# Optimization experiments

Measured on AMD Instinct MI355X. Metric: run time of the kernel, lower is better.

The kernel has to match this reference:

```python
import jax, jax.numpy as jnp
import numpy as np

B, S, H, NH = 1, 2048, 1024, 16
HD = H // NH
LAYER_NUMBER = 1
EPS = 1e-5
NEG_INF = -1e9


def _layernorm(x, g, b):
    mu = jnp.mean(x, axis=-1, keepdims=True)
    var = jnp.mean((x - mu) ** 2, axis=-1, keepdims=True)
    return (x - mu) * jax.lax.rsqrt(var + EPS) * g + b


def _bloom_gelu(x):
    # tanh approximation used by Megatron/Bloom
    return x * 0.5 * (1.0 + jnp.tanh(0.79788456 * x * (1.0 + 0.044715 * x * x)))


def setup_inputs() -> dict:
    key = jax.random.key(0)
    ks = jax.random.split(key, 8)

    def w(k, shape, scale=0.02):
        return jax.random.normal(k, shape, jnp.float32) * scale

    # additive causal mask: 0 where attended, -1e9 where masked
    causal = jnp.where(jnp.tril(jnp.ones((S, S), bool)), 0.0, NEG_INF).astype(jnp.float32)
    attention_mask = causal[None, None]  # [1,1,S,S]

    return {
        "hidden_states": jax.random.normal(ks[0], (B, S, H), jnp.float32),
        "attention_mask": attention_mask,
        "alibi": w(ks[1], (B * NH, 1, S), 1.0),
        "ln1_g": jnp.ones((H,), jnp.float32),
        "ln1_b": jnp.zeros((H,), jnp.float32),
        "qkv_w": w(ks[2], (3 * H, H)),
        "qkv_b": jnp.zeros((3 * H,), jnp.float32),
        "dense_w": w(ks[3], (H, H)),
        "dense_b": jnp.zeros((H,), jnp.float32),
        "ln2_g": jnp.ones((H,), jnp.float32),
        "ln2_b": jnp.zeros((H,), jnp.float32),
        "fc1_w": w(ks[4], (4 * H, H)),
        "fc1_b": jnp.zeros((4 * H,), jnp.float32),
        "fc2_w": w(ks[5], (H, 4 * H)),
        "fc2_b": jnp.zeros((H,), jnp.float32),
    }


def reference(hidden_states, attention_mask, alibi,
              ln1_g, ln1_b, qkv_w, qkv_b, dense_w, dense_b,
              ln2_g, ln2_b, fc1_w, fc1_b, fc2_w, fc2_b):
    dtype = hidden_states.dtype
    norm_factor = np.sqrt(HD).astype(np.float32) * LAYER_NUMBER
    beta = 1.0 / LAYER_NUMBER

    # --- input layernorm (residual = pre-LN hidden states) ---
    ln_out = _layernorm(hidden_states, ln1_g, ln1_b)
    residual = hidden_states

    # --- attention ---
    fused = ln_out @ qkv_w.T + qkv_b                      # [B,S,3H]
    fused = fused.reshape(B, S, NH, 3 * HD)
    q, k, v = fused[..., :HD], fused[..., HD:2 * HD], fused[..., 2 * HD:]

    scores = jnp.einsum('bqhd,bkhd->bhqk', q, k) / norm_factor \
             + beta * alibi.reshape(B, NH, 1, S)          # [B,NH,S,S]
    attn = scores * LAYER_NUMBER + attention_mask
    attn = jnp.maximum(attn, jnp.finfo(attn.dtype).min)
    probs = jax.nn.softmax(attn.astype(jnp.float32), axis=-1).astype(dtype)
    probs = probs * (attention_mask == 0.0)               # zero out masked positions

    ctx = jnp.einsum('bhqk,bkhd->bqhd', probs, v).reshape(B, S, H)
    attn_out = ctx @ dense_w.T + dense_b + residual       # dropout_add, p=0

    # --- post-attention layernorm + MLP ---
    ln2_out = _layernorm(attn_out, ln2_g, ln2_b)
    residual2 = attn_out
    h = _bloom_gelu(ln2_out @ fc1_w.T + fc1_b)            # [B,S,4H]
    out = h @ fc2_w.T + fc2_b + residual2                 # dropout_add, p=0
    return out
```

## Files before the change

kernel.cpp:

```cpp
#include <hip/hip_runtime.h>
#include <hip/hip_bf16.h>

typedef unsigned short u16;
typedef __attribute__((ext_vector_type(8))) short bf16x8;
typedef __attribute__((ext_vector_type(4))) float f32x4;

typedef __attribute__((address_space(1))) const void cgvoid;
typedef __attribute__((address_space(3))) void lvoid;

static __device__ __forceinline__ u16 f2bf(float x) {
    __hip_bfloat16 h = __float2bfloat16(x);
    return __builtin_bit_cast(u16, h);
}
static __device__ __forceinline__ float bf2f(u16 x) {
    return __builtin_bit_cast(float, ((unsigned)x) << 16);
}

static __device__ __forceinline__ void gload_lds16(const u16* g, u16* l) {
    __builtin_amdgcn_global_load_lds((cgvoid*)g, (lvoid*)l, 16, 0, 0);
}

__global__ __launch_bounds__(256) void prep(
    const float* __restrict__ hidden, const float* __restrict__ g1,
    const float* __restrict__ b1, u16* __restrict__ ln_out,
    const float* __restrict__ qkv_w, const float* __restrict__ dense_w,
    const float* __restrict__ fc1_w, const float* __restrict__ fc2_w,
    u16* __restrict__ qkv_wb, u16* __restrict__ dense_wb,
    u16* __restrict__ fc1_wb, u16* __restrict__ fc2_wb)
{
    const int t = threadIdx.x;
    if (blockIdx.x < 2048) {
        const int row = blockIdx.x;
        const float4 v = ((const float4*)(hidden + (size_t)row * 1024))[t];
        float s  = v.x + v.y + v.z + v.w;
        float sq = v.x*v.x + v.y*v.y + v.z*v.z + v.w*v.w;
#pragma unroll
        for (int d = 1; d < 64; d <<= 1) {
            s  += __shfl_xor(s, d, 64);
            sq += __shfl_xor(sq, d, 64);
        }
        __shared__ float ss[4], ssq[4];
        const int wave = t >> 6, lane = t & 63;
        if (lane == 0) { ss[wave] = s; ssq[wave] = sq; }
        __syncthreads();
        s  = ss[0] + ss[1] + ss[2] + ss[3];
        sq = ssq[0] + ssq[1] + ssq[2] + ssq[3];
        const float mu = s * (1.f / 1024.f);
        const float rinv = rsqrtf(sq * (1.f / 1024.f) - mu * mu + 1e-5f);
        const float4 gv = ((const float4*)g1)[t];
        const float4 bv = ((const float4*)b1)[t];
        ushort4 pk;
        pk.x = f2bf((v.x - mu) * rinv * gv.x + bv.x);
        pk.y = f2bf((v.y - mu) * rinv * gv.y + bv.y);
        pk.z = f2bf((v.z - mu) * rinv * gv.z + bv.z);
        pk.w = f2bf((v.w - mu) * rinv * gv.w + bv.w);
        ((ushort4*)(ln_out + (size_t)row * 1024))[t] = pk;
        return;
    }
    constexpr int C0 = 786432;
    constexpr int C1 = C0 + 262144;
    constexpr int C2 = C1 + 1048576;
    constexpr int C3 = C2 + 1048576;
    int i = (blockIdx.x - 2048) * 256 + t;
    const int stride = (gridDim.x - 2048) * 256;
    for (; i < C3; i += stride) {
        const float* src; u16* dst; int j;
        if (i < C0)      { src = qkv_w;   dst = qkv_wb;   j = i; }
        else if (i < C1) { src = dense_w; dst = dense_wb; j = i - C0; }
        else if (i < C2) { src = fc1_w;   dst = fc1_wb;   j = i - C1; }
        else             { src = fc2_w;   dst = fc2_wb;   j = i - C2; }
        const float4 v = ((const float4*)src)[j];
        ushort4 pk;
        pk.x = f2bf(v.x); pk.y = f2bf(v.y); pk.z = f2bf(v.z); pk.w = f2bf(v.w);
        ((ushort4*)dst)[j] = pk;
    }
}

template<int EPI, int BM, int BN>
__global__ __launch_bounds__(256, (BN == 128) ? 3 : 4) void gemm_bt(
    const u16* __restrict__ A, const u16* __restrict__ Bw,
    const float* __restrict__ bias, void* __restrict__ Cout,
    u16* __restrict__ p0, u16* __restrict__ pext,
    u16* __restrict__ kPo, u16* __restrict__ vPo,
    int M, int N, int K, int Kspan)
{
    constexpr int WC = BN / 64;
    constexpr int WR = 4 / WC;
    constexpr int MI = BM / (WR * 16);
    constexpr int NI = 4;
    __shared__ __align__(16) u16 As[BM * 64];
    __shared__ __align__(16) u16 Bs[BN * 64];
    const int t = threadIdx.x;
    const int lane = t & 63;
    const int wave = t >> 6;
    const int wr = wave / WC, wc = wave % WC;
    const int g = lane >> 4, r16 = lane & 15;

    const int nxy = gridDim.x * gridDim.y;
    const int bid0 = blockIdx.x + gridDim.x * blockIdx.y;
    const int v = (bid0 & 7) * (nxy >> 3) + (bid0 >> 3);
    const int tile_m = (v / gridDim.y) * BM;
    const int tile_n = (v % gridDim.y) * BN;
    const int kb = blockIdx.z * Kspan;

    f32x4 acc[MI][NI] = {};

    for (int k0 = kb; k0 < kb + Kspan; k0 += 64) {
        __syncthreads();
#pragma unroll
        for (int i = 0; i < BM / 32; ++i) {
            const int off = (t + i * 256) * 8;
            gload_lds16(A + (size_t)(tile_m + (off >> 6)) * K + k0 + (off & 63), As + off);
        }
#pragma unroll
        for (int i = 0; i < BN / 32; ++i) {
            const int off = (t + i * 256) * 8;
            gload_lds16(Bw + (size_t)(tile_n + (off >> 6)) * K + k0 + (off & 63), Bs + off);
        }
        __syncthreads();

        bf16x8 af[MI][2], bfr[NI][2];
#pragma unroll
        for (int mi = 0; mi < MI; ++mi)
#pragma unroll
            for (int ks = 0; ks < 2; ++ks)
                af[mi][ks] = *(const bf16x8*)(As + (wr*(MI*16) + mi*16 + r16)*64 + ks*32 + g*8);
#pragma unroll
        for (int ni = 0; ni < NI; ++ni)
#pragma unroll
            for (int ks = 0; ks < 2; ++ks)
                bfr[ni][ks] = *(const bf16x8*)(Bs + (wc*64 + ni*16 + r16)*64 + ks*32 + g*8);
#pragma unroll
        for (int mi = 0; mi < MI; ++mi)
#pragma unroll
            for (int ni = 0; ni < NI; ++ni) {
                acc[mi][ni] = __builtin_amdgcn_mfma_f32_16x16x32_bf16(af[mi][0], bfr[ni][0], acc[mi][ni], 0, 0, 0);
                acc[mi][ni] = __builtin_amdgcn_mfma_f32_16x16x32_bf16(af[mi][1], bfr[ni][1], acc[mi][ni], 0, 0, 0);
            }
    }

    u16* dst = nullptr;
    if constexpr (EPI == 4)
        dst = (blockIdx.z == 0) ? p0 : pext + (size_t)(blockIdx.z - 1) * ((size_t)M * N);

#pragma unroll
    for (int mi = 0; mi < MI; ++mi) {
#pragma unroll
        for (int ni = 0; ni < NI; ++ni) {
            const int col = tile_n + wc*64 + ni*16 + r16;
            const int row0 = tile_m + wr*(MI*16) + mi*16 + g*4;
            float vv[4];
#pragma unroll
            for (int r = 0; r < 4; ++r) {
                if constexpr (EPI == 4) vv[r] = acc[mi][ni][r];
                else                    vv[r] = acc[mi][ni][r] + bias[col];
            }
#pragma unroll
            for (int r = 0; r < 4; ++r) {
                const int row = row0 + r;
                if constexpr (EPI == 4) {
                    dst[(size_t)row * N + col] = f2bf(vv[r]);
                } else if constexpr (EPI == 0 || EPI == 3) {
                    ((u16*)Cout)[(size_t)row * N + col] = f2bf(vv[r]);
                } else {
                    const float c = 0.79788456f * vv[r] * (1.0f + 0.044715f * vv[r] * vv[r]);
                    ((u16*)Cout)[(size_t)row * N + col] = f2bf(vv[r] / (1.0f + __expf(-2.0f * c)));
                }
            }
            if constexpr (EPI == 3) {
                const int h = col / 192;
                const int fm = col % 192;
                if ((fm >> 6) == 1) {
                    const int f = fm - 64;
                    const int ks = f >> 5, gg = (f >> 3) & 3, e = f & 7;
#pragma unroll
                    for (int r = 0; r < 4; ++r) {
                        const int tkn = row0 + r;
                        const int kt = tkn >> 6, w = tkn & 63;
                        const int kn = ((w >> 5) << 1) | ((w >> 2) & 1);
                        const int rp = ((w >> 3) & 3) * 4 + (w & 3);
                        kPo[((size_t)(h*32 + kt))*4096 + (kn*2 + ks)*512 + (gg*16 + rp)*8 + e] = f2bf(vv[r]);
                    }
                } else if ((fm >> 6) == 2) {
                    const int f = fm - 128;
                    const int nd = f >> 4, rv = f & 15;
                    const int kt = row0 >> 6, w = row0 & 63;
                    const int ks = w >> 5, gg = (w >> 3) & 3, e0 = w & 7;
                    ushort4 pk4;
                    pk4.x = f2bf(vv[0]); pk4.y = f2bf(vv[1]);
                    pk4.z = f2bf(vv[2]); pk4.w = f2bf(vv[3]);
                    *(ushort4*)(vPo + ((size_t)(h*32 + kt))*4096 + (nd*2 + ks)*512 + (gg*16 + rv)*8 + e0) = pk4;
                }
            }
        }
    }
}

__global__ __launch_bounds__(256) void reduce2_ln(
    const u16* __restrict__ p0, const u16* __restrict__ p1,
    const float* __restrict__ bias, const float* __restrict__ res,
    float* __restrict__ attn_o, const float* __restrict__ g2,
    const float* __restrict__ b2, u16* __restrict__ ln_out)
{
    const int row = blockIdx.x;
    const int t = threadIdx.x;
    const size_t i = (size_t)row * 256 + t;
    const ushort4 a0 = ((const ushort4*)p0)[i];
    const ushort4 a1 = ((const ushort4*)p1)[i];
    const float4 bv = ((const float4*)bias)[t];
    const float4 rv = ((const float4*)res)[i];
    float4 v;
    v.x = bf2f(a0.x) + bf2f(a1.x) + bv.x + rv.x;
    v.y = bf2f(a0.y) + bf2f(a1.y) + bv.y + rv.y;
    v.z = bf2f(a0.z) + bf2f(a1.z) + bv.z + rv.z;
    v.w = bf2f(a0.w) + bf2f(a1.w) + bv.w + rv.w;
    ((float4*)attn_o)[i] = v;

    float s  = v.x + v.y + v.z + v.w;
    float sq = v.x*v.x + v.y*v.y + v.z*v.z + v.w*v.w;
#pragma unroll
    for (int d = 1; d < 64; d <<= 1) {
        s  += __shfl_xor(s, d, 64);
        sq += __shfl_xor(sq, d, 64);
    }
    __shared__ float ss[4], ssq[4];
    const int wave = t >> 6, lane = t & 63;
    if (lane == 0) { ss[wave] = s; ssq[wave] = sq; }
    __syncthreads();
    s  = ss[0] + ss[1] + ss[2] + ss[3];
    sq = ssq[0] + ssq[1] + ssq[2] + ssq[3];
    const float mu = s * (1.f / 1024.f);
    const float rinv = rsqrtf(sq * (1.f / 1024.f) - mu * mu + 1e-5f);
    const float4 gv = ((const float4*)g2)[t];
    const float4 b2v = ((const float4*)b2)[t];
    ushort4 pk;
    pk.x = f2bf((v.x - mu) * rinv * gv.x + b2v.x);
    pk.y = f2bf((v.y - mu) * rinv * gv.y + b2v.y);
    pk.z = f2bf((v.z - mu) * rinv * gv.z + b2v.z);
    pk.w = f2bf((v.w - mu) * rinv * gv.w + b2v.w);
    ((ushort4*)(ln_out + (size_t)row * 1024))[t] = pk;
}

template<int NP>
__global__ __launch_bounds__(256) void reduce_bias_res(
    const u16* __restrict__ p0, const u16* __restrict__ pext,
    const float* __restrict__ bias, const float* __restrict__ res,
    float* __restrict__ out, int n4, int n4row)
{
    int i = blockIdx.x * blockDim.x + threadIdx.x;
    const int stride = gridDim.x * blockDim.x;
    for (; i < n4; i += stride) {
        const ushort4 a0 = ((const ushort4*)p0)[i];
        float ax = bf2f(a0.x), ay = bf2f(a0.y), az = bf2f(a0.z), aw = bf2f(a0.w);
#pragma unroll
        for (int j = 0; j < NP - 1; ++j) {
            const ushort4 b = ((const ushort4*)pext)[(size_t)j * n4 + i];
            ax += bf2f(b.x); ay += bf2f(b.y); az += bf2f(b.z); aw += bf2f(b.w);
        }
        const float4 bv = ((const float4*)bias)[i & (n4row - 1)];
        const float4 rv = ((const float4*)res)[i];
        float4 o;
        o.x = ax + bv.x + rv.x;
        o.y = ay + bv.y + rv.y;
        o.z = az + bv.z + rv.z;
        o.w = aw + bv.w + rv.w;
        ((float4*)out)[i] = o;
    }
}

__global__ __launch_bounds__(256, 4) void attn_swapped(
    const u16* __restrict__ fused, const u16* __restrict__ kP,
    const u16* __restrict__ vP, const float* __restrict__ alibi,
    u16* __restrict__ ctx)
{
    const int bid = blockIdx.x;
    const int h = bid & 15;
    const int qt = 127 - (bid >> 4);
    const int qw0 = qt * 16;
    const int t = threadIdx.x;
    const int lane = t & 63, wave = t >> 6;
    const int g = lane >> 4, r16 = lane & 15;
    const int qrow = qw0 + r16;

    __shared__ float Ms[4][16], Ls[4][16];
    __shared__ float Os[4][4][16][17];

    const u16* qbase = fused + (size_t)qrow * 3072 + h * 192;
    bf16x8 qf[2];
    qf[0] = *(const bf16x8*)(qbase + g*8);
    qf[1] = *(const bf16x8*)(qbase + 32 + g*8);

    f32x4 o_acc[4] = {};
    float m_r = -3.0e38f, l_r = 0.f;

    const u16* kPh = kP + (size_t)h * 32 * 4096;
    const u16* vPh = vP + (size_t)h * 32 * 4096;
    const float* abase = alibi + (size_t)h * 2048;

    const int nkt = (qw0 >> 6) + 1;
    for (int kt = wave; kt < nkt; kt += 4) {
        const int kt0 = kt * 64;
        const u16* kT = kPh + (size_t)kt * 4096;
        const u16* vT = vPh + (size_t)kt * 4096;

        bf16x8 kf[4][2], vf[4][2];
#pragma unroll
        for (int kn = 0; kn < 4; ++kn) {
            kf[kn][0] = *(const bf16x8*)(kT + (kn*2 + 0)*512 + lane*8);
            kf[kn][1] = *(const bf16x8*)(kT + (kn*2 + 1)*512 + lane*8);
        }
        float4 al[4];
#pragma unroll
        for (int kn = 0; kn < 4; ++kn)
            al[kn] = *(const float4*)(abase + kt0 + 32*(kn>>1) + 8*g + 4*(kn&1));
#pragma unroll
        for (int nd = 0; nd < 4; ++nd) {
            vf[nd][0] = *(const bf16x8*)(vT + (nd*2 + 0)*512 + lane*8);
            vf[nd][1] = *(const bf16x8*)(vT + (nd*2 + 1)*512 + lane*8);
        }

        f32x4 sc[4] = {};
#pragma unroll
        for (int kn = 0; kn < 4; ++kn) {
            sc[kn] = __builtin_amdgcn_mfma_f32_16x16x32_bf16(kf[kn][0], qf[0], sc[kn], 0, 0, 0);
            sc[kn] = __builtin_amdgcn_mfma_f32_16x16x32_bf16(kf[kn][1], qf[1], sc[kn], 0, 0, 0);
        }

        float s[4][4];
        float rmax = -3.0e38f;
#pragma unroll
        for (int kn = 0; kn < 4; ++kn) {
            const int kb = kt0 + 32*(kn>>1) + 8*g + 4*(kn&1);
            const float alv[4] = {al[kn].x, al[kn].y, al[kn].z, al[kn].w};
#pragma unroll
            for (int r = 0; r < 4; ++r) {
                float v = sc[kn][r] * 0.125f + alv[r];
                v = (kb + r <= qrow) ? v : -1.0e30f;
                s[kn][r] = v;
                rmax = fmaxf(rmax, v);
            }
        }
        rmax = fmaxf(rmax, __shfl_xor(rmax, 16, 64));
        rmax = fmaxf(rmax, __shfl_xor(rmax, 32, 64));

        const float mnew = fmaxf(m_r, rmax);
        const float scale = __expf(m_r - mnew);
        m_r = mnew;

        float psum = 0.f;
        u16 ph[4][4];
#pragma unroll
        for (int kn = 0; kn < 4; ++kn)
#pragma unroll
            for (int r = 0; r < 4; ++r) {
                const float p = __expf(s[kn][r] - mnew);
                psum += p;
                ph[kn][r] = f2bf(p);
            }
        psum += __shfl_xor(psum, 16, 64);
        psum += __shfl_xor(psum, 32, 64);
        l_r = l_r * scale + psum;

#pragma unroll
        for (int nd = 0; nd < 4; ++nd)
#pragma unroll
            for (int r = 0; r < 4; ++r)
                o_acc[nd][r] *= scale;

        bf16x8 pf[2];
#pragma unroll
        for (int ks = 0; ks < 2; ++ks) {
            union { bf16x8 v; u16 e[8]; } u;
#pragma unroll
            for (int r = 0; r < 4; ++r) { u.e[r] = ph[2*ks][r]; u.e[4+r] = ph[2*ks+1][r]; }
            pf[ks] = u.v;
        }
#pragma unroll
        for (int nd = 0; nd < 4; ++nd) {
            o_acc[nd] = __builtin_amdgcn_mfma_f32_16x16x32_bf16(vf[nd][0], pf[0], o_acc[nd], 0, 0, 0);
            o_acc[nd] = __builtin_amdgcn_mfma_f32_16x16x32_bf16(vf[nd][1], pf[1], o_acc[nd], 0, 0, 0);
        }
    }

#pragma unroll
    for (int nd = 0; nd < 4; ++nd)
#pragma unroll
        for (int r = 0; r < 4; ++r)
            Os[wave][nd][g*4 + r][r16] = o_acc[nd][r];
    if (g == 0) { Ms[wave][r16] = m_r; Ls[wave][r16] = l_r; }
    __syncthreads();

    if (wave == 0) {
        const float m0 = Ms[0][r16], m1 = Ms[1][r16], m2 = Ms[2][r16], m3 = Ms[3][r16];
        const float ms = fmaxf(fmaxf(m0, m1), fmaxf(m2, m3));
        const float f0 = __expf(m0 - ms), f1 = __expf(m1 - ms);
        const float f2 = __expf(m2 - ms), f3 = __expf(m3 - ms);
        const float l = f0*Ls[0][r16] + f1*Ls[1][r16] + f2*Ls[2][r16] + f3*Ls[3][r16];
        const float inv = 1.0f / l;
#pragma unroll
        for (int nd = 0; nd < 4; ++nd) {
            float v[4];
#pragma unroll
            for (int r = 0; r < 4; ++r) {
                const int d = g*4 + r;
                v[r] = (f0*Os[0][nd][d][r16] + f1*Os[1][nd][d][r16] +
                        f2*Os[2][nd][d][r16] + f3*Os[3][nd][d][r16]) * inv;
            }
            ushort4 pk;
            pk.x = f2bf(v[0]); pk.y = f2bf(v[1]); pk.z = f2bf(v[2]); pk.w = f2bf(v[3]);
            *(ushort4*)(ctx + (size_t)qrow * 1024 + h*64 + nd*16 + g*4) = pk;
        }
    }
}

extern "C" void kernel_launch(void* const* d_in, const int* in_sizes, int n_in,
                              void* d_out, int out_size, void* d_ws, size_t ws_size,
                              hipStream_t stream)
{
    (void)in_sizes; (void)n_in; (void)out_size; (void)ws_size;
    const float* hidden  = (const float*)d_in[0];
    const float* alibi   = (const float*)d_in[2];
    const float* ln1_g   = (const float*)d_in[3];
    const float* ln1_b   = (const float*)d_in[4];
    const float* qkv_w   = (const float*)d_in[5];
    const float* qkv_b   = (const float*)d_in[6];
    const float* dense_w = (const float*)d_in[7];
    const float* dense_b = (const float*)d_in[8];
    const float* ln2_g   = (const float*)d_in[9];
    const float* ln2_b   = (const float*)d_in[10];
    const float* fc1_w   = (const float*)d_in[11];
    const float* fc1_b   = (const float*)d_in[12];
    const float* fc2_w   = (const float*)d_in[13];
    const float* fc2_b   = (const float*)d_in[14];
    float* out = (float*)d_out;

    char* p = (char*)d_ws;
    u16* ln_buf   = (u16*)p;  p += (size_t)2048 * 1024 * 2;
    u16* qkv_wb   = (u16*)p;  p += (size_t)3072 * 1024 * 2;
    u16* fusedq   = (u16*)p;  p += (size_t)2048 * 3072 * 2;
    u16* ctx      = (u16*)p;  p += (size_t)2048 * 1024 * 2;
    u16* dense_wb = (u16*)p;  p += (size_t)1024 * 1024 * 2;
    float* attn_o = (float*)p; p += (size_t)2048 * 1024 * 4;
    u16* fc1_wb   = (u16*)p;  p += (size_t)4096 * 1024 * 2;
    u16* fc2_wb   = (u16*)p;  p += (size_t)1024 * 4096 * 2;
    u16* pext     = (u16*)p;  p += (size_t)3 * 2048 * 1024 * 2;
    u16* part0    = (u16*)p;  p += (size_t)2048 * 1024 * 2;
    u16* hbuf = fusedq;
    u16* kP = (u16*)attn_o;
    u16* vP = kP + (size_t)16 * 32 * 4096;

    prep<<<6144, 256, 0, stream>>>(hidden, ln1_g, ln1_b, ln_buf,
                                   qkv_w, dense_w, fc1_w, fc2_w,
                                   qkv_wb, dense_wb, fc1_wb, fc2_wb);
    gemm_bt<3,128,64><<<dim3(16, 48), 256, 0, stream>>>(ln_buf, qkv_wb, qkv_b, fusedq,
                                                        nullptr, nullptr, kP, vP,
                                                        2048, 3072, 1024, 1024);
    attn_swapped<<<2048, 256, 0, stream>>>(fusedq, kP, vP, alibi, ctx);
    gemm_bt<4,128,64><<<dim3(16, 16, 2), 256, 0, stream>>>(ctx, dense_wb, nullptr, nullptr,
                                                           part0, pext, nullptr, nullptr,
                                                           2048, 1024, 1024, 512);
    reduce2_ln<<<2048, 256, 0, stream>>>(part0, pext, dense_b, hidden, attn_o,
                                         ln2_g, ln2_b, ln_buf);
    gemm_bt<2,128,128><<<dim3(16, 32), 256, 0, stream>>>(ln_buf, fc1_wb, fc1_b, hbuf,
                                                         nullptr, nullptr, nullptr, nullptr,
                                                         2048, 4096, 1024, 1024);
    gemm_bt<4,128,128><<<dim3(16, 8, 4), 256, 0, stream>>>(hbuf, fc2_wb, nullptr, nullptr,
                                                           part0, pext, nullptr, nullptr,
                                                           2048, 1024, 4096, 1024);
    reduce_bias_res<4><<<2048, 256, 0, stream>>>(part0, pext, fc2_b, attn_o, out,
                                                 2048*1024/4, 256);
}
```

Before: 157.4 us.

## Pair causal query tiles per attention block and pre-pack Q fragments

The attention kernel now handles two 16-row query tiles per block, one from the long end and one from the short end of the causal triangle, so every block does about the same work and the grid is halved. The QKV GEMM epilogue no longer writes the full fused row-major output. It scatters Q into an MFMA-fragment-packed layout, as K and V already were, so each Q fragment is read as one contiguous 16-byte load per lane and the dead fused Q/K/V store is gone. In exchange each block runs serially over both tiles with two extra syncthreads, and the epilogue's Q stores become scattered 2-byte writes.

```diff
diff --git a/kernel.cpp b/kernel.cpp
--- a/kernel.cpp
+++ b/kernel.cpp
@@ -81,7 +81,7 @@
     const u16* __restrict__ A, const u16* __restrict__ Bw,
     const float* __restrict__ bias, void* __restrict__ Cout,
     u16* __restrict__ p0, u16* __restrict__ pext,
-    u16* __restrict__ kPo, u16* __restrict__ vPo,
+    u16* __restrict__ qPo, u16* __restrict__ kPo, u16* __restrict__ vPo,
     int M, int N, int K, int Kspan)
 {
     constexpr int WC = BN / 64;
@@ -155,22 +155,32 @@
                 if constexpr (EPI == 4) vv[r] = acc[mi][ni][r];
                 else                    vv[r] = acc[mi][ni][r] + bias[col];
             }
-#pragma unroll
-            for (int r = 0; r < 4; ++r) {
-                const int row = row0 + r;
-                if constexpr (EPI == 4) {
-                    dst[(size_t)row * N + col] = f2bf(vv[r]);
-                } else if constexpr (EPI == 0 || EPI == 3) {
-                    ((u16*)Cout)[(size_t)row * N + col] = f2bf(vv[r]);
-                } else {
-                    const float c = 0.79788456f * vv[r] * (1.0f + 0.044715f * vv[r] * vv[r]);
-                    ((u16*)Cout)[(size_t)row * N + col] = f2bf(vv[r] / (1.0f + __expf(-2.0f * c)));
+            if constexpr (EPI != 3) {
+#pragma unroll
+                for (int r = 0; r < 4; ++r) {
+                    const int row = row0 + r;
+                    if constexpr (EPI == 4) {
+                        dst[(size_t)row * N + col] = f2bf(vv[r]);
+                    } else if constexpr (EPI == 0) {
+                        ((u16*)Cout)[(size_t)row * N + col] = f2bf(vv[r]);
+                    } else {
+                        const float c = 0.79788456f * vv[r] * (1.0f + 0.044715f * vv[r] * vv[r]);
+                        ((u16*)Cout)[(size_t)row * N + col] = f2bf(vv[r] / (1.0f + __expf(-2.0f * c)));
+                    }
                 }
-            }
-            if constexpr (EPI == 3) {
+            } else {
                 const int h = col / 192;
                 const int fm = col % 192;
-                if ((fm >> 6) == 1) {
+                if ((fm >> 6) == 0) {
+                    const int f = fm;
+                    const int ks = f >> 5, gg = (f >> 3) & 3, e = f & 7;
+#pragma unroll
+                    for (int r = 0; r < 4; ++r) {
+                        const int tkn = row0 + r;
+                        const int qt = tkn >> 4, rr = tkn & 15;
+                        qPo[((size_t)(h*128 + qt)*2 + ks)*512 + (gg*16 + rr)*8 + e] = f2bf(vv[r]);
+                    }
+                } else if ((fm >> 6) == 1) {
                     const int f = fm - 64;
                     const int ks = f >> 5, gg = (f >> 3) & 3, e = f & 7;
 #pragma unroll
@@ -181,7 +191,7 @@
                         const int rp = ((w >> 3) & 3) * 4 + (w & 3);
                         kPo[((size_t)(h*32 + kt))*4096 + (kn*2 + ks)*512 + (gg*16 + rp)*8 + e] = f2bf(vv[r]);
                     }
-                } else if ((fm >> 6) == 2) {
+                } else {
                     const int f = fm - 128;
                     const int nd = f >> 4, rv = f & 15;
                     const int kt = row0 >> 6, w = row0 & 63;
@@ -269,146 +279,151 @@
 }
 
 __global__ __launch_bounds__(256, 4) void attn_swapped(
-    const u16* __restrict__ fused, const u16* __restrict__ kP,
+    const u16* __restrict__ qP, const u16* __restrict__ kP,
     const u16* __restrict__ vP, const float* __restrict__ alibi,
     u16* __restrict__ ctx)
 {
     const int bid = blockIdx.x;
     const int h = bid & 15;
-    const int qt = 127 - (bid >> 4);
-    const int qw0 = qt * 16;
+    const int b = bid >> 4;
     const int t = threadIdx.x;
     const int lane = t & 63, wave = t >> 6;
     const int g = lane >> 4, r16 = lane & 15;
-    const int qrow = qw0 + r16;
 
     __shared__ float Ms[4][16], Ls[4][16];
     __shared__ float Os[4][4][16][17];
-
-    const u16* qbase = fused + (size_t)qrow * 3072 + h * 192;
-    bf16x8 qf[2];
-    qf[0] = *(const bf16x8*)(qbase + g*8);
-    qf[1] = *(const bf16x8*)(qbase + 32 + g*8);
-
-    f32x4 o_acc[4] = {};
-    float m_r = -3.0e38f, l_r = 0.f;
 
     const u16* kPh = kP + (size_t)h * 32 * 4096;
     const u16* vPh = vP + (size_t)h * 32 * 4096;
     const float* abase = alibi + (size_t)h * 2048;
 
-    const int nkt = (qw0 >> 6) + 1;
-    for (int kt = wave; kt < nkt; kt += 4) {
-        const int kt0 = kt * 64;
-        const u16* kT = kPh + (size_t)kt * 4096;
-        const u16* vT = vPh + (size_t)kt * 4096;
-
-        bf16x8 kf[4][2], vf[4][2];
-#pragma unroll
-        for (int kn = 0; kn < 4; ++kn) {
-            kf[kn][0] = *(const bf16x8*)(kT + (kn*2 + 0)*512 + lane*8);
-            kf[kn][1] = *(const bf16x8*)(kT + (kn*2 + 1)*512 + lane*8);
-        }
-        float4 al[4];
-#pragma unroll
-        for (int kn = 0; kn < 4; ++kn)
-            al[kn] = *(const float4*)(abase + kt0 + 32*(kn>>1) + 8*g + 4*(kn&1));
-#pragma unroll
-        for (int nd = 0; nd < 4; ++nd) {
-            vf[nd][0] = *(const bf16x8*)(vT + (nd*2 + 0)*512 + lane*8);
-            vf[nd][1] = *(const bf16x8*)(vT + (nd*2 + 1)*512 + lane*8);
-        }
-
-        f32x4 sc[4] = {};
-#pragma unroll
-        for (int kn = 0; kn < 4; ++kn) {
-            sc[kn] = __builtin_amdgcn_mfma_f32_16x16x32_bf16(kf[kn][0], qf[0], sc[kn], 0, 0, 0);
-            sc[kn] = __builtin_amdgcn_mfma_f32_16x16x32_bf16(kf[kn][1], qf[1], sc[kn], 0, 0, 0);
-        }
-
-        float s[4][4];
-        float rmax = -3.0e38f;
-#pragma unroll
-        for (int kn = 0; kn < 4; ++kn) {
-            const int kb = kt0 + 32*(kn>>1) + 8*g + 4*(kn&1);
-            const float alv[4] = {al[kn].x, al[kn].y, al[kn].z, al[kn].w};
-#pragma unroll
-            for (int r = 0; r < 4; ++r) {
-                float v = sc[kn][r] * 0.125f + alv[r];
-                v = (kb + r <= qrow) ? v : -1.0e30f;
-                s[kn][r] = v;
-                rmax = fmaxf(rmax, v);
-            }
-        }
-        rmax = fmaxf(rmax, __shfl_xor(rmax, 16, 64));
-        rmax = fmaxf(rmax, __shfl_xor(rmax, 32, 64));
-
-        const float mnew = fmaxf(m_r, rmax);
-        const float scale = __expf(m_r - mnew);
-        m_r = mnew;
-
-        float psum = 0.f;
-        u16 ph[4][4];
-#pragma unroll
-        for (int kn = 0; kn < 4; ++kn)
-#pragma unroll
-            for (int r = 0; r < 4; ++r) {
-                const float p = __expf(s[kn][r] - mnew);
-                psum += p;
-                ph[kn][r] = f2bf(p);
-            }
-        psum += __shfl_xor(psum, 16, 64);
-        psum += __shfl_xor(psum, 32, 64);
-        l_r = l_r * scale + psum;
-
+#pragma unroll
+    for (int half = 0; half < 2; ++half) {
+        const int qt = half ? b : (127 - b);
+        const int qw0 = qt * 16;
+        const int qrow = qw0 + r16;
+
+        bf16x8 qf[2];
+        qf[0] = *(const bf16x8*)(qP + ((size_t)(h*128 + qt)*2 + 0)*512 + lane*8);
+        qf[1] = *(const bf16x8*)(qP + ((size_t)(h*128 + qt)*2 + 1)*512 + lane*8);
+
+        f32x4 o_acc[4] = {};
+        float m_r = -3.0e38f, l_r = 0.f;
+
+        const int nkt = (qw0 >> 6) + 1;
+        for (int kt = wave; kt < nkt; kt += 4) {
+            const int kt0 = kt * 64;
+            const u16* kT = kPh + (size_t)kt * 4096;
+            const u16* vT = vPh + (size_t)kt * 4096;
+
+            bf16x8 kf[4][2], vf[4][2];
+#pragma unroll
+            for (int kn = 0; kn < 4; ++kn) {
+                kf[kn][0] = *(const bf16x8*)(kT + (kn*2 + 0)*512 + lane*8);
+                kf[kn][1] = *(const bf16x8*)(kT + (kn*2 + 1)*512 + lane*8);
+            }
+            float4 al[4];
+#pragma unroll
+            for (int kn = 0; kn < 4; ++kn)
+                al[kn] = *(const float4*)(abase + kt0 + 32*(kn>>1) + 8*g + 4*(kn&1));
+#pragma unroll
+            for (int nd = 0; nd < 4; ++nd) {
+                vf[nd][0] = *(const bf16x8*)(vT + (nd*2 + 0)*512 + lane*8);
+                vf[nd][1] = *(const bf16x8*)(vT + (nd*2 + 1)*512 + lane*8);
+            }
+
+            f32x4 sc[4] = {};
+#pragma unroll
+            for (int kn = 0; kn < 4; ++kn) {
+                sc[kn] = __builtin_amdgcn_mfma_f32_16x16x32_bf16(kf[kn][0], qf[0], sc[kn], 0, 0, 0);
+                sc[kn] = __builtin_amdgcn_mfma_f32_16x16x32_bf16(kf[kn][1], qf[1], sc[kn], 0, 0, 0);
+            }
+
+            float s[4][4];
+            float rmax = -3.0e38f;
+#pragma unroll
+            for (int kn = 0; kn < 4; ++kn) {
+                const int kb = kt0 + 32*(kn>>1) + 8*g + 4*(kn&1);
+                const float alv[4] = {al[kn].x, al[kn].y, al[kn].z, al[kn].w};
+#pragma unroll
+                for (int r = 0; r < 4; ++r) {
+                    float v = sc[kn][r] * 0.125f + alv[r];
+                    v = (kb + r <= qrow) ? v : -1.0e30f;
+                    s[kn][r] = v;
+                    rmax = fmaxf(rmax, v);
+                }
+            }
+            rmax = fmaxf(rmax, __shfl_xor(rmax, 16, 64));
+            rmax = fmaxf(rmax, __shfl_xor(rmax, 32, 64));
+
+            const float mnew = fmaxf(m_r, rmax);
+            const float scale = __expf(m_r - mnew);
+            m_r = mnew;
+
+            float psum = 0.f;
+            u16 ph[4][4];
+#pragma unroll
+            for (int kn = 0; kn < 4; ++kn)
+#pragma unroll
+                for (int r = 0; r < 4; ++r) {
+                    const float p = __expf(s[kn][r] - mnew);
+                    psum += p;
+                    ph[kn][r] = f2bf(p);
+                }
+            psum += __shfl_xor(psum, 16, 64);
+            psum += __shfl_xor(psum, 32, 64);
+            l_r = l_r * scale + psum;
+
+#pragma unroll
+            for (int nd = 0; nd < 4; ++nd)
+#pragma unroll
+                for (int r = 0; r < 4; ++r)
+                    o_acc[nd][r] *= scale;
+
+            bf16x8 pf[2];
+#pragma unroll
+            for (int ks = 0; ks < 2; ++ks) {
+                union { bf16x8 v; u16 e[8]; } u;
+#pragma unroll
+                for (int r = 0; r < 4; ++r) { u.e[r] = ph[2*ks][r]; u.e[4+r] = ph[2*ks+1][r]; }
+                pf[ks] = u.v;
+            }
+#pragma unroll
+            for (int nd = 0; nd < 4; ++nd) {
+                o_acc[nd] = __builtin_amdgcn_mfma_f32_16x16x32_bf16(vf[nd][0], pf[0], o_acc[nd], 0, 0, 0);
+                o_acc[nd] = __builtin_amdgcn_mfma_f32_16x16x32_bf16(vf[nd][1], pf[1], o_acc[nd], 0, 0, 0);
+            }
+        }
+
+        __syncthreads();
 #pragma unroll
         for (int nd = 0; nd < 4; ++nd)
 #pragma unroll
             for (int r = 0; r < 4; ++r)
-                o_acc[nd][r] *= scale;
-
-        bf16x8 pf[2];
-#pragma unroll
-        for (int ks = 0; ks < 2; ++ks) {
-            union { bf16x8 v; u16 e[8]; } u;
-#pragma unroll
-            for (int r = 0; r < 4; ++r) { u.e[r] = ph[2*ks][r]; u.e[4+r] = ph[2*ks+1][r]; }
-            pf[ks] = u.v;
-        }
-#pragma unroll
-        for (int nd = 0; nd < 4; ++nd) {
-            o_acc[nd] = __builtin_amdgcn_mfma_f32_16x16x32_bf16(vf[nd][0], pf[0], o_acc[nd], 0, 0, 0);
-            o_acc[nd] = __builtin_amdgcn_mfma_f32_16x16x32_bf16(vf[nd][1], pf[1], o_acc[nd], 0, 0, 0);
-        }
-    }
-
-#pragma unroll
-    for (int nd = 0; nd < 4; ++nd)
-#pragma unroll
-        for (int r = 0; r < 4; ++r)
-            Os[wave][nd][g*4 + r][r16] = o_acc[nd][r];
-    if (g == 0) { Ms[wave][r16] = m_r; Ls[wave][r16] = l_r; }
-    __syncthreads();
-
-    if (wave == 0) {
-        const float m0 = Ms[0][r16], m1 = Ms[1][r16], m2 = Ms[2][r16], m3 = Ms[3][r16];
-        const float ms = fmaxf(fmaxf(m0, m1), fmaxf(m2, m3));
-        const float f0 = __expf(m0 - ms), f1 = __expf(m1 - ms);
-        const float f2 = __expf(m2 - ms), f3 = __expf(m3 - ms);
-        const float l = f0*Ls[0][r16] + f1*Ls[1][r16] + f2*Ls[2][r16] + f3*Ls[3][r16];
-        const float inv = 1.0f / l;
-#pragma unroll
-        for (int nd = 0; nd < 4; ++nd) {
-            float v[4];
-#pragma unroll
-            for (int r = 0; r < 4; ++r) {
-                const int d = g*4 + r;
-                v[r] = (f0*Os[0][nd][d][r16] + f1*Os[1][nd][d][r16] +
-                        f2*Os[2][nd][d][r16] + f3*Os[3][nd][d][r16]) * inv;
-            }
-            ushort4 pk;
-            pk.x = f2bf(v[0]); pk.y = f2bf(v[1]); pk.z = f2bf(v[2]); pk.w = f2bf(v[3]);
-            *(ushort4*)(ctx + (size_t)qrow * 1024 + h*64 + nd*16 + g*4) = pk;
+                Os[wave][nd][g*4 + r][r16] = o_acc[nd][r];
+        if (g == 0) { Ms[wave][r16] = m_r; Ls[wave][r16] = l_r; }
+        __syncthreads();
+
+        if (wave == 0) {
+            const float m0 = Ms[0][r16], m1 = Ms[1][r16], m2 = Ms[2][r16], m3 = Ms[3][r16];
+            const float ms = fmaxf(fmaxf(m0, m1), fmaxf(m2, m3));
+            const float f0 = __expf(m0 - ms), f1 = __expf(m1 - ms);
+            const float f2 = __expf(m2 - ms), f3 = __expf(m3 - ms);
+            const float l = f0*Ls[0][r16] + f1*Ls[1][r16] + f2*Ls[2][r16] + f3*Ls[3][r16];
+            const float inv = 1.0f / l;
+#pragma unroll
+            for (int nd = 0; nd < 4; ++nd) {
+                float v[4];
+#pragma unroll
+                for (int r = 0; r < 4; ++r) {
+                    const int d = g*4 + r;
+                    v[r] = (f0*Os[0][nd][d][r16] + f1*Os[1][nd][d][r16] +
+                            f2*Os[2][nd][d][r16] + f3*Os[3][nd][d][r16]) * inv;
+                }
+                ushort4 pk;
+                pk.x = f2bf(v[0]); pk.y = f2bf(v[1]); pk.z = f2bf(v[2]); pk.w = f2bf(v[3]);
+                *(ushort4*)(ctx + (size_t)qrow * 1024 + h*64 + nd*16 + g*4) = pk;
+            }
         }
     }
 }
@@ -437,7 +452,7 @@
     char* p = (char*)d_ws;
     u16* ln_buf   = (u16*)p;  p += (size_t)2048 * 1024 * 2;
     u16* qkv_wb   = (u16*)p;  p += (size_t)3072 * 1024 * 2;
-    u16* fusedq   = (u16*)p;  p += (size_t)2048 * 3072 * 2;
+    u16* qP       = (u16*)p;  p += (size_t)2048 * 3072 * 2;
     u16* ctx      = (u16*)p;  p += (size_t)2048 * 1024 * 2;
     u16* dense_wb = (u16*)p;  p += (size_t)1024 * 1024 * 2;
     float* attn_o = (float*)p; p += (size_t)2048 * 1024 * 4;
@@ -445,27 +460,27 @@
     u16* fc2_wb   = (u16*)p;  p += (size_t)1024 * 4096 * 2;
     u16* pext     = (u16*)p;  p += (size_t)3 * 2048 * 1024 * 2;
     u16* part0    = (u16*)p;  p += (size_t)2048 * 1024 * 2;
-    u16* hbuf = fusedq;
+    u16* hbuf = qP;
     u16* kP = (u16*)attn_o;
     u16* vP = kP + (size_t)16 * 32 * 4096;
 
     prep<<<6144, 256, 0, stream>>>(hidden, ln1_g, ln1_b, ln_buf,
                                    qkv_w, dense_w, fc1_w, fc2_w,
                                    qkv_wb, dense_wb, fc1_wb, fc2_wb);
-    gemm_bt<3,128,64><<<dim3(16, 48), 256, 0, stream>>>(ln_buf, qkv_wb, qkv_b, fusedq,
-                                                        nullptr, nullptr, kP, vP,
+    gemm_bt<3,128,64><<<dim3(16, 48), 256, 0, stream>>>(ln_buf, qkv_wb, qkv_b, nullptr,
+                                                        nullptr, nullptr, qP, kP, vP,
                                                         2048, 3072, 1024, 1024);
-    attn_swapped<<<2048, 256, 0, stream>>>(fusedq, kP, vP, alibi, ctx);
+    attn_swapped<<<1024, 256, 0, stream>>>(qP, kP, vP, alibi, ctx);
     gemm_bt<4,128,64><<<dim3(16, 16, 2), 256, 0, stream>>>(ctx, dense_wb, nullptr, nullptr,
-                                                           part0, pext, nullptr, nullptr,
+                                                           part0, pext, nullptr, nullptr, nullptr,
                                                            2048, 1024, 1024, 512);
     reduce2_ln<<<2048, 256, 0, stream>>>(part0, pext, dense_b, hidden, attn_o,
                                          ln2_g, ln2_b, ln_buf);
     gemm_bt<2,128,128><<<dim3(16, 32), 256, 0, stream>>>(ln_buf, fc1_wb, fc1_b, hbuf,
-                                                         nullptr, nullptr, nullptr, nullptr,
+                                                         nullptr, nullptr, nullptr, nullptr, nullptr,
                                                          2048, 4096, 1024, 1024);
     gemm_bt<4,128,128><<<dim3(16, 8, 4), 256, 0, stream>>>(hbuf, fc2_wb, nullptr, nullptr,
-                                                           part0, pext, nullptr, nullptr,
+                                                           part0, pext, nullptr, nullptr, nullptr,
                                                            2048, 1024, 4096, 1024);
     reduce_bias_res<4><<<2048, 256, 0, stream>>>(part0, pext, fc2_b, attn_o, out,
                                                  2048*1024/4, 256);
```

After: 162.6 us. 1.03x slower.
